# Kernel tuning notes

Measured on AMD Instinct MI355X. Metric: run time of the kernel, lower is better.

## Reference

```python
import jax, jax.numpy as jnp
import numpy as np

EPSILON = 1e-7  # wl-coref utils.add_dummy epsilon
LEAKY_SLOPE = 0.01  # torch.nn.LeakyReLU default

N_MENTIONS = 10000
BATCH = 512
N_ANTS = 50
MENTION_EMB = 1024
PW_EMB = 64
IN_FEATURES = 3 * MENTION_EMB + PW_EMB  # 3136
HIDDEN = 128


def setup_inputs() -> dict:
    key = jax.random.key(0)
    ks = jax.random.split(key, 9)
    return {
        "all_mentions": jax.random.normal(ks[0], (N_MENTIONS, MENTION_EMB), jnp.float32),
        "mentions_batch": jax.random.normal(ks[1], (BATCH, MENTION_EMB), jnp.float32),
        "pw_batch": jax.random.normal(ks[2], (BATCH, N_ANTS, PW_EMB), jnp.float32),
        "top_indices_batch": jax.random.randint(ks[3], (BATCH, N_ANTS), 0, N_MENTIONS, jnp.int64 if jax.config.jax_enable_x64 else jnp.int32),
        "top_rough_scores_batch": jax.random.normal(ks[4], (BATCH, N_ANTS), jnp.float32),
        "W1": jax.random.normal(ks[5], (IN_FEATURES, HIDDEN), jnp.float32) * 0.02,
        "b1": jax.random.normal(ks[6], (HIDDEN,), jnp.float32) * 0.02,
        "W_out": jax.random.normal(ks[7], (HIDDEN, 1), jnp.float32) * 0.02,
        "b_out": jax.random.normal(ks[8], (1,), jnp.float32) * 0.02,
    }


def reference(all_mentions, mentions_batch, pw_batch, top_indices_batch,
              top_rough_scores_batch, W1, b1, W_out, b_out):
    batch, n_ants = top_indices_batch.shape
    emb = mentions_batch.shape[1]
    # pair matrix: [batch, n_ants, 3*emb + pw_emb]
    a_mentions = jnp.broadcast_to(mentions_batch[:, None, :], (batch, n_ants, emb))
    b_mentions = all_mentions[top_indices_batch]          # gather: [batch, n_ants, emb]
    similarity = a_mentions * b_mentions
    pair_matrix = jnp.concatenate((a_mentions, b_mentions, similarity, pw_batch), axis=2)
    # FFNN: Linear -> LeakyReLU -> (Dropout=identity in eval) -> Linear(out=1)
    h = jax.nn.leaky_relu(jnp.einsum('baf,fh->bah', pair_matrix, W1) + b1, LEAKY_SLOPE)
    ffnn = (jnp.einsum('bah,ho->bao', h, W_out) + b_out)[..., 0]  # [batch, n_ants]
    scores = top_rough_scores_batch + ffnn
    # add_dummy(eps=True): prepend a column of EPSILON
    dummy = jnp.full((batch, 1), EPSILON, dtype=scores.dtype)
    return jnp.concatenate((dummy, scores), axis=1)  # [batch, n_ants + 1]
```

## Files before the change

kernel.cpp:

```cpp
#include <hip/hip_runtime.h>

#define N_MENT   10000
#define BATCH    512
#define N_ANTS   50
#define EMB      1024
#define PW_EMB   64
#define IN_F     3136
#define HID      128
#define M_TOT    (BATCH * N_ANTS)
#define EPS_VAL  1e-7f
#define SLOPE    0.01f

#define NKT      98
#define CONV_BLK 196
#define MAIN_BLK (M_TOT / 32)

using f32x4 = __attribute__((ext_vector_type(4))) float;
using s16x8 = __attribute__((ext_vector_type(8))) short;
using u16x8 = __attribute__((ext_vector_type(8))) unsigned short;

__device__ __forceinline__ unsigned short f2bf(float f) {
  unsigned u = __builtin_bit_cast(unsigned, f);
  u += 0x7FFFu + ((u >> 16) & 1u);
  return (unsigned short)(u >> 16);
}

__device__ __forceinline__ u16x8 pack8(float4 lo, float4 hi) {
  union { u16x8 v; unsigned u[4]; } r;
  asm("v_cvt_pk_bf16_f32 %0, %1, %2" : "=v"(r.u[0]) : "v"(lo.x), "v"(lo.y));
  asm("v_cvt_pk_bf16_f32 %0, %1, %2" : "=v"(r.u[1]) : "v"(lo.z), "v"(lo.w));
  asm("v_cvt_pk_bf16_f32 %0, %1, %2" : "=v"(r.u[2]) : "v"(hi.x), "v"(hi.y));
  asm("v_cvt_pk_bf16_f32 %0, %1, %2" : "=v"(r.u[3]) : "v"(hi.z), "v"(hi.w));
  return r.v;
}

__device__ __forceinline__ int tile_orig_k(int tk) {
  if (tk >= 96) return 3072 + (tk - 96) * 32;
  const int c = tk / 6, r = tk % 6;
  return (r >> 1) * 1024 + c * 64 + (r & 1) * 32;
}

__global__ __launch_bounds__(256) void k_convert(const float* __restrict__ w1,
                                                 unsigned short* __restrict__ w1f) {
  const int id   = blockIdx.x * 256 + threadIdx.x;
  const int lane = id & 63;
  const int tile = id >> 6;
  const int tk   = tile % NKT, tn = tile / NKT;
  const int n    = tn * 16 + (lane & 15);
  const int k    = tile_orig_k(tk) + (lane >> 4) * 8;
  u16x8 o;
  #pragma unroll
  for (int j = 0; j < 8; ++j) o[j] = f2bf(w1[(size_t)(k + j) * HID + n]);
  *(u16x8*)(w1f + (size_t)id * 8) = o;
}

__global__ __launch_bounds__(256) void k_main(
    const float* __restrict__ all_m, const float* __restrict__ men,
    const float* __restrict__ pw, const int* __restrict__ topi,
    const float* __restrict__ rough, const unsigned short* __restrict__ w1f,
    const float* __restrict__ b1, const float* __restrict__ wout,
    const float* __restrict__ bout, float* __restrict__ out) {
  __shared__ __align__(16) unsigned short Xs[2][3][32 * 72];
  __shared__ float red[4 * 32];

  const int t  = threadIdx.x;
  const int m0 = blockIdx.x * 32;

  const int sr = t >> 3, sq = t & 7;
  const int m  = m0 + sr;
  const int bb = m / N_ANTS;
  const int bidx = topi[m];
  const float* pA = men   + (size_t)bb   * EMB    + sq * 8;
  const float* pB = all_m + (size_t)bidx * EMB    + sq * 8;
  const float* pP = pw    + (size_t)m    * PW_EMB + sq * 8;

  const int lane = t & 63, wid = t >> 6;
  const int ln = lane & 15, lg = lane >> 4;
  const int wcol = wid * 32;
  const unsigned short* wfA = w1f + ((size_t)(2 * wid)     * NKT) * 512 + lane * 8;
  const unsigned short* wfB = w1f + ((size_t)(2 * wid + 1) * NKT) * 512 + lane * 8;

  f32x4 acc[2][2] = {};

  float4 a0 = ((const float4*)pA)[0], a1 = ((const float4*)pA)[1];
  float4 b0 = ((const float4*)pB)[0], b1v = ((const float4*)pB)[1];

  int buf = 0;
  for (int c = 0; c < 16; ++c) {
    s16x8 wr[12];
    #pragma unroll
    for (int j6 = 0; j6 < 6; ++j6) {
      wr[j6 * 2]     = *(const s16x8*)(wfA + (size_t)(c * 6 + j6) * 512);
      wr[j6 * 2 + 1] = *(const s16x8*)(wfB + (size_t)(c * 6 + j6) * 512);
    }

    *(u16x8*)&Xs[buf][0][sr * 72 + sq * 8] = pack8(a0, a1);
    *(u16x8*)&Xs[buf][1][sr * 72 + sq * 8] = pack8(b0, b1v);
    float4 s0 = make_float4(a0.x * b0.x,  a0.y * b0.y,  a0.z * b0.z,  a0.w * b0.w);
    float4 s1 = make_float4(a1.x * b1v.x, a1.y * b1v.y, a1.z * b1v.z, a1.w * b1v.w);
    *(u16x8*)&Xs[buf][2][sr * 72 + sq * 8] = pack8(s0, s1);

    if (c < 15) {
      const float* qA = pA + (c + 1) * 64;
      const float* qB = pB + (c + 1) * 64;
      a0 = ((const float4*)qA)[0]; a1 = ((const float4*)qA)[1];
      b0 = ((const float4*)qB)[0]; b1v = ((const float4*)qB)[1];
    } else {
      a0 = ((const float4*)pP)[0]; a1 = ((const float4*)pP)[1];
    }

    __syncthreads();
    #pragma unroll
    for (int j6 = 0; j6 < 6; ++j6) {
      const int reg = j6 >> 1, ks = j6 & 1;
      s16x8 x0 = *(const s16x8*)&Xs[buf][reg][ln * 72        + ks * 32 + lg * 8];
      s16x8 x1 = *(const s16x8*)&Xs[buf][reg][(16 + ln) * 72 + ks * 32 + lg * 8];
      acc[0][0] = __builtin_amdgcn_mfma_f32_16x16x32_bf16(x0, wr[j6 * 2],     acc[0][0], 0, 0, 0);
      acc[0][1] = __builtin_amdgcn_mfma_f32_16x16x32_bf16(x0, wr[j6 * 2 + 1], acc[0][1], 0, 0, 0);
      acc[1][0] = __builtin_amdgcn_mfma_f32_16x16x32_bf16(x1, wr[j6 * 2],     acc[1][0], 0, 0, 0);
      acc[1][1] = __builtin_amdgcn_mfma_f32_16x16x32_bf16(x1, wr[j6 * 2 + 1], acc[1][1], 0, 0, 0);
    }
    buf ^= 1;
  }

  {
    s16x8 wr[4];
    #pragma unroll
    for (int ks = 0; ks < 2; ++ks) {
      wr[ks * 2]     = *(const s16x8*)(wfA + (size_t)(96 + ks) * 512);
      wr[ks * 2 + 1] = *(const s16x8*)(wfB + (size_t)(96 + ks) * 512);
    }
    *(u16x8*)&Xs[buf][0][sr * 72 + sq * 8] = pack8(a0, a1);
    __syncthreads();
    #pragma unroll
    for (int ks = 0; ks < 2; ++ks) {
      s16x8 x0 = *(const s16x8*)&Xs[buf][0][ln * 72        + ks * 32 + lg * 8];
      s16x8 x1 = *(const s16x8*)&Xs[buf][0][(16 + ln) * 72 + ks * 32 + lg * 8];
      acc[0][0] = __builtin_amdgcn_mfma_f32_16x16x32_bf16(x0, wr[ks * 2],     acc[0][0], 0, 0, 0);
      acc[0][1] = __builtin_amdgcn_mfma_f32_16x16x32_bf16(x0, wr[ks * 2 + 1], acc[0][1], 0, 0, 0);
      acc[1][0] = __builtin_amdgcn_mfma_f32_16x16x32_bf16(x1, wr[ks * 2],     acc[1][0], 0, 0, 0);
      acc[1][1] = __builtin_amdgcn_mfma_f32_16x16x32_bf16(x1, wr[ks * 2 + 1], acc[1][1], 0, 0, 0);
    }
  }

  const int n0 = wcol + ln, n1 = wcol + 16 + ln;
  const float bias0 = b1[n0], bias1 = b1[n1];
  const float w_0 = wout[n0], w_1 = wout[n1];
  #pragma unroll
  for (int mf = 0; mf < 2; ++mf)
    #pragma unroll
    for (int e = 0; e < 4; ++e) {
      const int ml = mf * 16 + lg * 4 + e;
      float h0 = acc[mf][0][e] + bias0;
      float h1 = acc[mf][1][e] + bias1;
      h0 = h0 > 0.f ? h0 : SLOPE * h0;
      h1 = h1 > 0.f ? h1 : SLOPE * h1;
      float ss = h0 * w_0 + h1 * w_1;
      ss += __shfl_xor(ss, 1);
      ss += __shfl_xor(ss, 2);
      ss += __shfl_xor(ss, 4);
      ss += __shfl_xor(ss, 8);
      if (ln == 0) red[wid * 32 + ml] = ss;
    }
  __syncthreads();
  if (t < 32) {
    const int gm = m0 + t;
    const int gb = gm / N_ANTS;
    const int ga = gm - gb * N_ANTS;
    out[(size_t)gb * (N_ANTS + 1) + 1 + ga] =
        rough[gm] + red[t] + red[32 + t] + red[64 + t] + red[96 + t] + bout[0];
  }
  if (t == 0) {
    for (int g = m0 / N_ANTS; g <= (m0 + 31) / N_ANTS; ++g)
      out[(size_t)g * (N_ANTS + 1)] = EPS_VAL;
  }
}

__global__ void k_eps(float* __restrict__ out) {
  out[(size_t)threadIdx.x * (N_ANTS + 1)] = EPS_VAL;
}

__global__ __launch_bounds__(128) void k_fb(const float* __restrict__ all_m,
                                            const float* __restrict__ men,
                                            const float* __restrict__ pw,
                                            const int*   __restrict__ topi,
                                            const float* __restrict__ rough,
                                            const float* __restrict__ w1,
                                            const float* __restrict__ b1,
                                            const float* __restrict__ wout,
                                            const float* __restrict__ bout,
                                            float* __restrict__ out) {
  __shared__ float xs[IN_F];
  __shared__ float hred[HID];
  const int pair = blockIdx.x;
  const int t = threadIdx.x;
  const int bb = pair / N_ANTS;
  const int idx = topi[pair];
  const float* pA = men + (size_t)bb * EMB;
  const float* pB = all_m + (size_t)idx * EMB;
  for (int k = t; k < EMB; k += 128) {
    float a = pA[k], b = pB[k];
    xs[k] = a; xs[EMB + k] = b; xs[2 * EMB + k] = a * b;
  }
  if (t < PW_EMB) xs[3 * EMB + t] = pw[(size_t)pair * PW_EMB + t];
  __syncthreads();
  float acc = 0.f;
  for (int k = 0; k < IN_F; ++k) acc = fmaf(xs[k], w1[(size_t)k * HID + t], acc);
  acc += b1[t];
  acc = acc > 0.f ? acc : SLOPE * acc;
  hred[t] = acc * wout[t];
  __syncthreads();
  for (int off = 64; off > 0; off >>= 1) {
    if (t < off) hred[t] += hred[t + off];
    __syncthreads();
  }
  if (t == 0)
    out[(size_t)bb * (N_ANTS + 1) + 1 + (pair - bb * N_ANTS)] = rough[pair] + hred[0] + bout[0];
}

extern "C" void kernel_launch(void* const* d_in, const int* in_sizes, int n_in,
                              void* d_out, int out_size, void* d_ws, size_t ws_size,
                              hipStream_t stream) {
  const float* all_m = (const float*)d_in[0];
  const float* men   = (const float*)d_in[1];
  const float* pw    = (const float*)d_in[2];
  const int*   topi  = (const int*)  d_in[3];
  const float* rough = (const float*)d_in[4];
  const float* w1    = (const float*)d_in[5];
  const float* b1    = (const float*)d_in[6];
  const float* wout  = (const float*)d_in[7];
  const float* bout  = (const float*)d_in[8];
  float* out = (float*)d_out;

  const size_t W1F_BYTES = (size_t)HID * IN_F * sizeof(unsigned short);

  if (ws_size >= W1F_BYTES) {
    unsigned short* w1f = (unsigned short*)d_ws;
    k_convert<<<CONV_BLK, 256, 0, stream>>>(w1, w1f);
    k_main<<<MAIN_BLK, 256, 0, stream>>>(all_m, men, pw, topi, rough, w1f,
                                         b1, wout, bout, out);
  } else {
    k_eps<<<1, BATCH, 0, stream>>>(out);
    k_fb<<<M_TOT, 128, 0, stream>>>(all_m, men, pw, topi, rough, w1, b1, wout, bout, out);
  }
}
```

Baseline: 54.85 us.

## Feed MFMA B operand directly from registers, dropping LDS staging and barriers

Restructures the main kernel so each wave loads its own 16 pair rows straight into registers in the MFMA operand layout, instead of staging converted activations through double-buffered shared memory with a block barrier every chunk. Waves are split two ways on M and two ways on N (four 16-column weight tiles each), with weights as the A operand, so the epilogue reduces across lane groups with two shuffles. This removes the LDS writes and reads and the per-iteration __syncthreads. In exchange each wave loads twice as much weight data per chunk, and activation loads are duplicated across the two N-halves.

```diff
diff --git a/kernel.cpp b/kernel.cpp
--- a/kernel.cpp
+++ b/kernel.cpp
@@ -25,14 +25,19 @@
   return (unsigned short)(u >> 16);
 }
 
-__device__ __forceinline__ u16x8 pack8(float4 lo, float4 hi) {
-  union { u16x8 v; unsigned u[4]; } r;
+__device__ __forceinline__ s16x8 pack8(float4 lo, float4 hi) {
+  union { s16x8 v; unsigned u[4]; } r;
   asm("v_cvt_pk_bf16_f32 %0, %1, %2" : "=v"(r.u[0]) : "v"(lo.x), "v"(lo.y));
   asm("v_cvt_pk_bf16_f32 %0, %1, %2" : "=v"(r.u[1]) : "v"(lo.z), "v"(lo.w));
   asm("v_cvt_pk_bf16_f32 %0, %1, %2" : "=v"(r.u[2]) : "v"(hi.x), "v"(hi.y));
   asm("v_cvt_pk_bf16_f32 %0, %1, %2" : "=v"(r.u[3]) : "v"(hi.z), "v"(hi.w));
   return r.v;
 }
+
+__device__ __forceinline__ float4 fmul4(float4 a, float4 b) {
+  return make_float4(a.x * b.x, a.y * b.y, a.z * b.z, a.w * b.w);
+}
+__device__ __forceinline__ float lky(float h) { return h > 0.f ? h : SLOPE * h; }
 
 __device__ __forceinline__ int tile_orig_k(int tk) {
   if (tk >= 96) return 3072 + (tk - 96) * 32;
@@ -60,115 +65,113 @@
     const float* __restrict__ rough, const unsigned short* __restrict__ w1f,
     const float* __restrict__ b1, const float* __restrict__ wout,
     const float* __restrict__ bout, float* __restrict__ out) {
-  __shared__ __align__(16) unsigned short Xs[2][3][32 * 72];
-  __shared__ float red[4 * 32];
-
-  const int t  = threadIdx.x;
-  const int m0 = blockIdx.x * 32;
-
-  const int sr = t >> 3, sq = t & 7;
-  const int m  = m0 + sr;
-  const int bb = m / N_ANTS;
-  const int bidx = topi[m];
-  const float* pA = men   + (size_t)bb   * EMB    + sq * 8;
-  const float* pB = all_m + (size_t)bidx * EMB    + sq * 8;
-  const float* pP = pw    + (size_t)m    * PW_EMB + sq * 8;
-
+  __shared__ float red[64];
+
+  const int t    = threadIdx.x;
   const int lane = t & 63, wid = t >> 6;
-  const int ln = lane & 15, lg = lane >> 4;
-  const int wcol = wid * 32;
-  const unsigned short* wfA = w1f + ((size_t)(2 * wid)     * NKT) * 512 + lane * 8;
-  const unsigned short* wfB = w1f + ((size_t)(2 * wid + 1) * NKT) * 512 + lane * 8;
-
-  f32x4 acc[2][2] = {};
-
-  float4 a0 = ((const float4*)pA)[0], a1 = ((const float4*)pA)[1];
-  float4 b0 = ((const float4*)pB)[0], b1v = ((const float4*)pB)[1];
-
-  int buf = 0;
+  const int ln   = lane & 15, lg = lane >> 4;
+  const int mg   = wid & 1, nh = wid >> 1;
+  const int m0   = blockIdx.x * 32;
+
+  const int mrow = m0 + mg * 16 + ln;
+  const int bb   = mrow / N_ANTS;
+  const int bidx = topi[mrow];
+  const float* pa = men   + (size_t)bb   * EMB    + lg * 8;
+  const float* pb = all_m + (size_t)bidx * EMB    + lg * 8;
+  const float* pp = pw    + (size_t)mrow * PW_EMB + lg * 8;
+
+  const unsigned short* wp0 = w1f + (size_t)(nh * 4 + 0) * NKT * 512 + lane * 8;
+  const unsigned short* wp1 = w1f + (size_t)(nh * 4 + 1) * NKT * 512 + lane * 8;
+  const unsigned short* wp2 = w1f + (size_t)(nh * 4 + 2) * NKT * 512 + lane * 8;
+  const unsigned short* wp3 = w1f + (size_t)(nh * 4 + 3) * NKT * 512 + lane * 8;
+
+  f32x4 acc[4] = {};
+
+  float4 ca0 = ((const float4*)pa)[0],        ca1 = ((const float4*)pa)[1];
+  float4 ca2 = ((const float4*)(pa + 32))[0], ca3 = ((const float4*)(pa + 32))[1];
+  float4 cb0 = ((const float4*)pb)[0],        cb1 = ((const float4*)pb)[1];
+  float4 cb2 = ((const float4*)(pb + 32))[0], cb3 = ((const float4*)(pb + 32))[1];
+
   for (int c = 0; c < 16; ++c) {
-    s16x8 wr[12];
+    float4 na0, na1, na2, na3, nb0, nb1, nb2, nb3;
+    if (c < 15) {
+      const float* qa = pa + (c + 1) * 64;
+      const float* qb = pb + (c + 1) * 64;
+      na0 = ((const float4*)qa)[0];        na1 = ((const float4*)qa)[1];
+      na2 = ((const float4*)(qa + 32))[0]; na3 = ((const float4*)(qa + 32))[1];
+      nb0 = ((const float4*)qb)[0];        nb1 = ((const float4*)qb)[1];
+      nb2 = ((const float4*)(qb + 32))[0]; nb3 = ((const float4*)(qb + 32))[1];
+    } else {
+      na0 = ((const float4*)pp)[0];        na1 = ((const float4*)pp)[1];
+      na2 = ((const float4*)(pp + 32))[0]; na3 = ((const float4*)(pp + 32))[1];
+      nb0 = na0; nb1 = na1; nb2 = na2; nb3 = na3;
+    }
+
+    s16x8 xf[6];
+    xf[0] = pack8(ca0, ca1);
+    xf[1] = pack8(ca2, ca3);
+    xf[2] = pack8(cb0, cb1);
+    xf[3] = pack8(cb2, cb3);
+    xf[4] = pack8(fmul4(ca0, cb0), fmul4(ca1, cb1));
+    xf[5] = pack8(fmul4(ca2, cb2), fmul4(ca3, cb3));
+
     #pragma unroll
-    for (int j6 = 0; j6 < 6; ++j6) {
-      wr[j6 * 2]     = *(const s16x8*)(wfA + (size_t)(c * 6 + j6) * 512);
-      wr[j6 * 2 + 1] = *(const s16x8*)(wfB + (size_t)(c * 6 + j6) * 512);
+    for (int j = 0; j < 6; ++j) {
+      const size_t off = (size_t)(c * 6 + j) * 512;
+      const s16x8 w0 = *(const s16x8*)(wp0 + off);
+      const s16x8 w1r = *(const s16x8*)(wp1 + off);
+      const s16x8 w2 = *(const s16x8*)(wp2 + off);
+      const s16x8 w3 = *(const s16x8*)(wp3 + off);
+      acc[0] = __builtin_amdgcn_mfma_f32_16x16x32_bf16(w0,  xf[j], acc[0], 0, 0, 0);
+      acc[1] = __builtin_amdgcn_mfma_f32_16x16x32_bf16(w1r, xf[j], acc[1], 0, 0, 0);
+      acc[2] = __builtin_amdgcn_mfma_f32_16x16x32_bf16(w2,  xf[j], acc[2], 0, 0, 0);
+      acc[3] = __builtin_amdgcn_mfma_f32_16x16x32_bf16(w3,  xf[j], acc[3], 0, 0, 0);
     }
-
-    *(u16x8*)&Xs[buf][0][sr * 72 + sq * 8] = pack8(a0, a1);
-    *(u16x8*)&Xs[buf][1][sr * 72 + sq * 8] = pack8(b0, b1v);
-    float4 s0 = make_float4(a0.x * b0.x,  a0.y * b0.y,  a0.z * b0.z,  a0.w * b0.w);
-    float4 s1 = make_float4(a1.x * b1v.x, a1.y * b1v.y, a1.z * b1v.z, a1.w * b1v.w);
-    *(u16x8*)&Xs[buf][2][sr * 72 + sq * 8] = pack8(s0, s1);
-
-    if (c < 15) {
-      const float* qA = pA + (c + 1) * 64;
-      const float* qB = pB + (c + 1) * 64;
-      a0 = ((const float4*)qA)[0]; a1 = ((const float4*)qA)[1];
-      b0 = ((const float4*)qB)[0]; b1v = ((const float4*)qB)[1];
-    } else {
-      a0 = ((const float4*)pP)[0]; a1 = ((const float4*)pP)[1];
-    }
-
-    __syncthreads();
-    #pragma unroll
-    for (int j6 = 0; j6 < 6; ++j6) {
-      const int reg = j6 >> 1, ks = j6 & 1;
-      s16x8 x0 = *(const s16x8*)&Xs[buf][reg][ln * 72        + ks * 32 + lg * 8];
-      s16x8 x1 = *(const s16x8*)&Xs[buf][reg][(16 + ln) * 72 + ks * 32 + lg * 8];
-      acc[0][0] = __builtin_amdgcn_mfma_f32_16x16x32_bf16(x0, wr[j6 * 2],     acc[0][0], 0, 0, 0);
-      acc[0][1] = __builtin_amdgcn_mfma_f32_16x16x32_bf16(x0, wr[j6 * 2 + 1], acc[0][1], 0, 0, 0);
-      acc[1][0] = __builtin_amdgcn_mfma_f32_16x16x32_bf16(x1, wr[j6 * 2],     acc[1][0], 0, 0, 0);
-      acc[1][1] = __builtin_amdgcn_mfma_f32_16x16x32_bf16(x1, wr[j6 * 2 + 1], acc[1][1], 0, 0, 0);
-    }
-    buf ^= 1;
+    ca0 = na0; ca1 = na1; ca2 = na2; ca3 = na3;
+    cb0 = nb0; cb1 = nb1; cb2 = nb2; cb3 = nb3;
   }
 
   {
-    s16x8 wr[4];
+    s16x8 xf0 = pack8(ca0, ca1);
+    s16x8 xf1 = pack8(ca2, ca3);
     #pragma unroll
     for (int ks = 0; ks < 2; ++ks) {
-      wr[ks * 2]     = *(const s16x8*)(wfA + (size_t)(96 + ks) * 512);
-      wr[ks * 2 + 1] = *(const s16x8*)(wfB + (size_t)(96 + ks) * 512);
+      const size_t off = (size_t)(96 + ks) * 512;
+      const s16x8 w0 = *(const s16x8*)(wp0 + off);
+      const s16x8 w1r = *(const s16x8*)(wp1 + off);
+      const s16x8 w2 = *(const s16x8*)(wp2 + off);
+      const s16x8 w3 = *(const s16x8*)(wp3 + off);
+      const s16x8 x = ks ? xf1 : xf0;
+      acc[0] = __builtin_amdgcn_mfma_f32_16x16x32_bf16(w0,  x, acc[0], 0, 0, 0);
+      acc[1] = __builtin_amdgcn_mfma_f32_16x16x32_bf16(w1r, x, acc[1], 0, 0, 0);
+      acc[2] = __builtin_amdgcn_mfma_f32_16x16x32_bf16(w2,  x, acc[2], 0, 0, 0);
+      acc[3] = __builtin_amdgcn_mfma_f32_16x16x32_bf16(w3,  x, acc[3], 0, 0, 0);
     }
-    *(u16x8*)&Xs[buf][0][sr * 72 + sq * 8] = pack8(a0, a1);
-    __syncthreads();
-    #pragma unroll
-    for (int ks = 0; ks < 2; ++ks) {
-      s16x8 x0 = *(const s16x8*)&Xs[buf][0][ln * 72        + ks * 32 + lg * 8];
-      s16x8 x1 = *(const s16x8*)&Xs[buf][0][(16 + ln) * 72 + ks * 32 + lg * 8];
-      acc[0][0] = __builtin_amdgcn_mfma_f32_16x16x32_bf16(x0, wr[ks * 2],     acc[0][0], 0, 0, 0);
-      acc[0][1] = __builtin_amdgcn_mfma_f32_16x16x32_bf16(x0, wr[ks * 2 + 1], acc[0][1], 0, 0, 0);
-      acc[1][0] = __builtin_amdgcn_mfma_f32_16x16x32_bf16(x1, wr[ks * 2],     acc[1][0], 0, 0, 0);
-      acc[1][1] = __builtin_amdgcn_mfma_f32_16x16x32_bf16(x1, wr[ks * 2 + 1], acc[1][1], 0, 0, 0);
-    }
-  }
-
-  const int n0 = wcol + ln, n1 = wcol + 16 + ln;
-  const float bias0 = b1[n0], bias1 = b1[n1];
-  const float w_0 = wout[n0], w_1 = wout[n1];
+  }
+
+  const float* b1p = b1   + nh * 64 + lg * 4;
+  const float* wop = wout + nh * 64 + lg * 4;
+  float ss = 0.f;
   #pragma unroll
-  for (int mf = 0; mf < 2; ++mf)
-    #pragma unroll
-    for (int e = 0; e < 4; ++e) {
-      const int ml = mf * 16 + lg * 4 + e;
-      float h0 = acc[mf][0][e] + bias0;
-      float h1 = acc[mf][1][e] + bias1;
-      h0 = h0 > 0.f ? h0 : SLOPE * h0;
-      h1 = h1 > 0.f ? h1 : SLOPE * h1;
-      float ss = h0 * w_0 + h1 * w_1;
-      ss += __shfl_xor(ss, 1);
-      ss += __shfl_xor(ss, 2);
-      ss += __shfl_xor(ss, 4);
-      ss += __shfl_xor(ss, 8);
-      if (ln == 0) red[wid * 32 + ml] = ss;
-    }
+  for (int nj = 0; nj < 4; ++nj) {
+    const float4 bv = *(const float4*)(b1p + nj * 16);
+    const float4 wv = *(const float4*)(wop + nj * 16);
+    ss = fmaf(lky(acc[nj][0] + bv.x), wv.x, ss);
+    ss = fmaf(lky(acc[nj][1] + bv.y), wv.y, ss);
+    ss = fmaf(lky(acc[nj][2] + bv.z), wv.z, ss);
+    ss = fmaf(lky(acc[nj][3] + bv.w), wv.w, ss);
+  }
+  ss += __shfl_xor(ss, 16);
+  ss += __shfl_xor(ss, 32);
+  if (lane < 16) red[wid * 16 + lane] = ss;
   __syncthreads();
   if (t < 32) {
-    const int gm = m0 + t;
-    const int gb = gm / N_ANTS;
-    const int ga = gm - gb * N_ANTS;
-    out[(size_t)gb * (N_ANTS + 1) + 1 + ga] =
-        rough[gm] + red[t] + red[32 + t] + red[64 + t] + red[96 + t] + bout[0];
+    const int mgq = t >> 4, ml = t & 15;
+    const int gm = m0 + mgq * 16 + ml;
+    const float val = red[mgq * 16 + ml] + red[(mgq + 2) * 16 + ml]
+                    + rough[gm] + bout[0];
+    const int gb = gm / N_ANTS, ga = gm - gb * N_ANTS;
+    out[(size_t)gb * (N_ANTS + 1) + 1 + ga] = val;
   }
   if (t == 0) {
     for (int g = m0 / N_ANTS; g <= (m0 + 31) / N_ANTS; ++g)
```

Result: slower. 97.21 us (+77.2%).

## Double threads per block, splitting hidden columns across eight waves

Applied to the files above, without the earlier changes.

The main kernel now runs 512 threads per block instead of 256. Each of eight waves owns 16 hidden columns instead of 32, and each thread stages 4 floats per row chunk instead of 8. This halves per-thread register use for weights and accumulators and raises wave-level parallelism for hiding gather latency. The cost is more barrier participants and a larger final cross-wave reduction, and each wave loads its own copy of the shared X tile fragments.

```diff
diff --git a/kernel.cpp b/kernel.cpp
--- a/kernel.cpp
+++ b/kernel.cpp
@@ -17,6 +17,7 @@
 
 using f32x4 = __attribute__((ext_vector_type(4))) float;
 using s16x8 = __attribute__((ext_vector_type(8))) short;
+using u16x4 = __attribute__((ext_vector_type(4))) unsigned short;
 using u16x8 = __attribute__((ext_vector_type(8))) unsigned short;
 
 __device__ __forceinline__ unsigned short f2bf(float f) {
@@ -25,13 +26,15 @@
   return (unsigned short)(u >> 16);
 }
 
-__device__ __forceinline__ u16x8 pack8(float4 lo, float4 hi) {
-  union { u16x8 v; unsigned u[4]; } r;
-  asm("v_cvt_pk_bf16_f32 %0, %1, %2" : "=v"(r.u[0]) : "v"(lo.x), "v"(lo.y));
-  asm("v_cvt_pk_bf16_f32 %0, %1, %2" : "=v"(r.u[1]) : "v"(lo.z), "v"(lo.w));
-  asm("v_cvt_pk_bf16_f32 %0, %1, %2" : "=v"(r.u[2]) : "v"(hi.x), "v"(hi.y));
-  asm("v_cvt_pk_bf16_f32 %0, %1, %2" : "=v"(r.u[3]) : "v"(hi.z), "v"(hi.w));
-  return r.v;
+__device__ __forceinline__ u16x4 pack4(float4 v) {
+  union { u16x4 o; unsigned u[2]; } r;
+  asm("v_cvt_pk_bf16_f32 %0, %1, %2" : "=v"(r.u[0]) : "v"(v.x), "v"(v.y));
+  asm("v_cvt_pk_bf16_f32 %0, %1, %2" : "=v"(r.u[1]) : "v"(v.z), "v"(v.w));
+  return r.o;
+}
+
+__device__ __forceinline__ float4 fmul4(float4 a, float4 b) {
+  return make_float4(a.x * b.x, a.y * b.y, a.z * b.z, a.w * b.w);
 }
 
 __device__ __forceinline__ int tile_orig_k(int tk) {
@@ -54,121 +57,105 @@
   *(u16x8*)(w1f + (size_t)id * 8) = o;
 }
 
-__global__ __launch_bounds__(256) void k_main(
+__global__ __launch_bounds__(512) void k_main(
     const float* __restrict__ all_m, const float* __restrict__ men,
     const float* __restrict__ pw, const int* __restrict__ topi,
     const float* __restrict__ rough, const unsigned short* __restrict__ w1f,
     const float* __restrict__ b1, const float* __restrict__ wout,
     const float* __restrict__ bout, float* __restrict__ out) {
   __shared__ __align__(16) unsigned short Xs[2][3][32 * 72];
-  __shared__ float red[4 * 32];
+  __shared__ float red[8 * 32];
 
   const int t  = threadIdx.x;
   const int m0 = blockIdx.x * 32;
 
-  const int sr = t >> 3, sq = t & 7;
+  const int sr = t >> 4, sq = t & 15;
   const int m  = m0 + sr;
   const int bb = m / N_ANTS;
   const int bidx = topi[m];
-  const float* pA = men   + (size_t)bb   * EMB    + sq * 8;
-  const float* pB = all_m + (size_t)bidx * EMB    + sq * 8;
-  const float* pP = pw    + (size_t)m    * PW_EMB + sq * 8;
+  const float* pA = men   + (size_t)bb   * EMB    + sq * 4;
+  const float* pB = all_m + (size_t)bidx * EMB    + sq * 4;
+  const float* pP = pw    + (size_t)m    * PW_EMB + sq * 4;
 
   const int lane = t & 63, wid = t >> 6;
   const int ln = lane & 15, lg = lane >> 4;
-  const int wcol = wid * 32;
-  const unsigned short* wfA = w1f + ((size_t)(2 * wid)     * NKT) * 512 + lane * 8;
-  const unsigned short* wfB = w1f + ((size_t)(2 * wid + 1) * NKT) * 512 + lane * 8;
-
-  f32x4 acc[2][2] = {};
-
-  float4 a0 = ((const float4*)pA)[0], a1 = ((const float4*)pA)[1];
-  float4 b0 = ((const float4*)pB)[0], b1v = ((const float4*)pB)[1];
+  const unsigned short* wf = w1f + (size_t)wid * NKT * 512 + lane * 8;
+
+  f32x4 acc[2] = {};
+
+  float4 av = ((const float4*)pA)[0];
+  float4 bv = ((const float4*)pB)[0];
 
   int buf = 0;
   for (int c = 0; c < 16; ++c) {
-    s16x8 wr[12];
-    #pragma unroll
-    for (int j6 = 0; j6 < 6; ++j6) {
-      wr[j6 * 2]     = *(const s16x8*)(wfA + (size_t)(c * 6 + j6) * 512);
-      wr[j6 * 2 + 1] = *(const s16x8*)(wfB + (size_t)(c * 6 + j6) * 512);
-    }
-
-    *(u16x8*)&Xs[buf][0][sr * 72 + sq * 8] = pack8(a0, a1);
-    *(u16x8*)&Xs[buf][1][sr * 72 + sq * 8] = pack8(b0, b1v);
-    float4 s0 = make_float4(a0.x * b0.x,  a0.y * b0.y,  a0.z * b0.z,  a0.w * b0.w);
-    float4 s1 = make_float4(a1.x * b1v.x, a1.y * b1v.y, a1.z * b1v.z, a1.w * b1v.w);
-    *(u16x8*)&Xs[buf][2][sr * 72 + sq * 8] = pack8(s0, s1);
+    *(u16x4*)&Xs[buf][0][sr * 72 + sq * 4] = pack4(av);
+    *(u16x4*)&Xs[buf][1][sr * 72 + sq * 4] = pack4(bv);
+    *(u16x4*)&Xs[buf][2][sr * 72 + sq * 4] = pack4(fmul4(av, bv));
 
     if (c < 15) {
-      const float* qA = pA + (c + 1) * 64;
-      const float* qB = pB + (c + 1) * 64;
-      a0 = ((const float4*)qA)[0]; a1 = ((const float4*)qA)[1];
-      b0 = ((const float4*)qB)[0]; b1v = ((const float4*)qB)[1];
+      av = ((const float4*)(pA + (c + 1) * 64))[0];
+      bv = ((const float4*)(pB + (c + 1) * 64))[0];
     } else {
-      a0 = ((const float4*)pP)[0]; a1 = ((const float4*)pP)[1];
-    }
+      av = ((const float4*)pP)[0];
+    }
+
+    s16x8 wr[6];
+    #pragma unroll
+    for (int j = 0; j < 6; ++j)
+      wr[j] = *(const s16x8*)(wf + (size_t)(c * 6 + j) * 512);
 
     __syncthreads();
     #pragma unroll
-    for (int j6 = 0; j6 < 6; ++j6) {
-      const int reg = j6 >> 1, ks = j6 & 1;
+    for (int j = 0; j < 6; ++j) {
+      const int reg = j >> 1, ks = j & 1;
       s16x8 x0 = *(const s16x8*)&Xs[buf][reg][ln * 72        + ks * 32 + lg * 8];
       s16x8 x1 = *(const s16x8*)&Xs[buf][reg][(16 + ln) * 72 + ks * 32 + lg * 8];
-      acc[0][0] = __builtin_amdgcn_mfma_f32_16x16x32_bf16(x0, wr[j6 * 2],     acc[0][0], 0, 0, 0);
-      acc[0][1] = __builtin_amdgcn_mfma_f32_16x16x32_bf16(x0, wr[j6 * 2 + 1], acc[0][1], 0, 0, 0);
-      acc[1][0] = __builtin_amdgcn_mfma_f32_16x16x32_bf16(x1, wr[j6 * 2],     acc[1][0], 0, 0, 0);
-      acc[1][1] = __builtin_amdgcn_mfma_f32_16x16x32_bf16(x1, wr[j6 * 2 + 1], acc[1][1], 0, 0, 0);
+      acc[0] = __builtin_amdgcn_mfma_f32_16x16x32_bf16(x0, wr[j], acc[0], 0, 0, 0);
+      acc[1] = __builtin_amdgcn_mfma_f32_16x16x32_bf16(x1, wr[j], acc[1], 0, 0, 0);
     }
     buf ^= 1;
   }
 
   {
-    s16x8 wr[4];
-    #pragma unroll
-    for (int ks = 0; ks < 2; ++ks) {
-      wr[ks * 2]     = *(const s16x8*)(wfA + (size_t)(96 + ks) * 512);
-      wr[ks * 2 + 1] = *(const s16x8*)(wfB + (size_t)(96 + ks) * 512);
-    }
-    *(u16x8*)&Xs[buf][0][sr * 72 + sq * 8] = pack8(a0, a1);
+    *(u16x4*)&Xs[buf][0][sr * 72 + sq * 4] = pack4(av);
+    s16x8 wr[2];
+    #pragma unroll
+    for (int ks = 0; ks < 2; ++ks)
+      wr[ks] = *(const s16x8*)(wf + (size_t)(96 + ks) * 512);
     __syncthreads();
     #pragma unroll
     for (int ks = 0; ks < 2; ++ks) {
       s16x8 x0 = *(const s16x8*)&Xs[buf][0][ln * 72        + ks * 32 + lg * 8];
       s16x8 x1 = *(const s16x8*)&Xs[buf][0][(16 + ln) * 72 + ks * 32 + lg * 8];
-      acc[0][0] = __builtin_amdgcn_mfma_f32_16x16x32_bf16(x0, wr[ks * 2],     acc[0][0], 0, 0, 0);
-      acc[0][1] = __builtin_amdgcn_mfma_f32_16x16x32_bf16(x0, wr[ks * 2 + 1], acc[0][1], 0, 0, 0);
-      acc[1][0] = __builtin_amdgcn_mfma_f32_16x16x32_bf16(x1, wr[ks * 2],     acc[1][0], 0, 0, 0);
-      acc[1][1] = __builtin_amdgcn_mfma_f32_16x16x32_bf16(x1, wr[ks * 2 + 1], acc[1][1], 0, 0, 0);
-    }
-  }
-
-  const int n0 = wcol + ln, n1 = wcol + 16 + ln;
-  const float bias0 = b1[n0], bias1 = b1[n1];
-  const float w_0 = wout[n0], w_1 = wout[n1];
+      acc[0] = __builtin_amdgcn_mfma_f32_16x16x32_bf16(x0, wr[ks], acc[0], 0, 0, 0);
+      acc[1] = __builtin_amdgcn_mfma_f32_16x16x32_bf16(x1, wr[ks], acc[1], 0, 0, 0);
+    }
+  }
+
+  const int n0 = wid * 16 + ln;
+  const float bias = b1[n0], w_o = wout[n0];
   #pragma unroll
   for (int mf = 0; mf < 2; ++mf)
     #pragma unroll
     for (int e = 0; e < 4; ++e) {
-      const int ml = mf * 16 + lg * 4 + e;
-      float h0 = acc[mf][0][e] + bias0;
-      float h1 = acc[mf][1][e] + bias1;
-      h0 = h0 > 0.f ? h0 : SLOPE * h0;
-      h1 = h1 > 0.f ? h1 : SLOPE * h1;
-      float ss = h0 * w_0 + h1 * w_1;
+      float h = acc[mf][e] + bias;
+      h = h > 0.f ? h : SLOPE * h;
+      float ss = h * w_o;
       ss += __shfl_xor(ss, 1);
       ss += __shfl_xor(ss, 2);
       ss += __shfl_xor(ss, 4);
       ss += __shfl_xor(ss, 8);
-      if (ln == 0) red[wid * 32 + ml] = ss;
+      if (ln == 0) red[wid * 32 + mf * 16 + lg * 4 + e] = ss;
     }
   __syncthreads();
   if (t < 32) {
     const int gm = m0 + t;
+    float v = red[t];
+    #pragma unroll
+    for (int w = 1; w < 8; ++w) v += red[w * 32 + t];
     const int gb = gm / N_ANTS;
     const int ga = gm - gb * N_ANTS;
-    out[(size_t)gb * (N_ANTS + 1) + 1 + ga] =
-        rough[gm] + red[t] + red[32 + t] + red[64 + t] + red[96 + t] + bout[0];
+    out[(size_t)gb * (N_ANTS + 1) + 1 + ga] = rough[gm] + v + bout[0];
   }
   if (t == 0) {
     for (int g = m0 / N_ANTS; g <= (m0 + 31) / N_ANTS; ++g)
@@ -237,7 +224,7 @@
   if (ws_size >= W1F_BYTES) {
     unsigned short* w1f = (unsigned short*)d_ws;
     k_convert<<<CONV_BLK, 256, 0, stream>>>(w1, w1f);
-    k_main<<<MAIN_BLK, 256, 0, stream>>>(all_m, men, pw, topi, rough, w1f,
+    k_main<<<MAIN_BLK, 512, 0, stream>>>(all_m, men, pw, topi, rough, w1f,
                                          b1, wout, bout, out);
   } else {
     k_eps<<<1, BATCH, 0, stream>>>(out);
```

Result: no change. 54.30 us (-1.0%).
